# Kernel optimization log

Hardware: AMD Instinct MI355X
Metric: run time of the kernel (lower is better)

Reference implementation:

```python
import jax, jax.numpy as jnp
import numpy as np

B, E, H, A = 16384, 128, 256, 20


def _xavier(key, shape):
    scale = (2.0 / (shape[0] + shape[1])) ** 0.5
    return (jax.random.normal(key, shape, jnp.float32) * scale).astype(jnp.float32)


def setup_inputs() -> dict:
    key = jax.random.key(0)
    ks = jax.random.split(key, 16)
    d = {
        'x1': jax.random.normal(ks[0], (B, E), jnp.float32),
        'x2': jax.random.normal(ks[1], (B, A, E), jnp.float32),
        'h': jax.random.normal(ks[2], (B, H), jnp.float32),
        'c1': jax.random.normal(ks[3], (B, H), jnp.float32),
        'c2': jax.random.normal(ks[4], (B, H), jnp.float32),
    }
    gate_names = ['f', 'i', 'c', 'o']
    for j, n in enumerate(gate_names):
        d[f'W1_{n}'] = _xavier(ks[5 + 2 * j], (H + E, H))
        d[f'W2_{n}'] = _xavier(ks[6 + 2 * j], (H + E, H))
        d[f'b1_{n}'] = jnp.zeros((H,), jnp.float32)
        d[f'b2_{n}'] = jnp.zeros((H,), jnp.float32)
    d['W_attn'] = _xavier(ks[13], (H + 2 * E, 1))
    return d


def reference(x1, x2, h, c1, c2,
              W1_f, W2_f, b1_f, b2_f,
              W1_i, W2_i, b1_i, b2_i,
              W1_c, W2_c, b1_c, b2_c,
              W1_o, W2_o, b1_o, b2_o,
              W_attn):
    hx1 = jnp.concatenate([h, x1], axis=1)                    # [B, H+E]
    # attention: score_a = [h, x1, x2_a] @ W_attn ; split W_attn to vectorize
    base = hx1 @ W_attn[:H + E, 0]                            # [B]
    scores = base[:, None] + jnp.einsum('bae,e->ba', x2, W_attn[H + E:, 0])  # [B, A]
    attn = jax.nn.softmax(scores, axis=1)
    x2m = jnp.einsum('ba,bae->be', attn, x2)                  # [B, E]
    hx2 = jnp.concatenate([h, x2m], axis=1)                   # [B, H+E]

    f1 = jax.nn.sigmoid(hx1 @ W1_f + b1_f)
    f2 = jax.nn.sigmoid(hx2 @ W2_f + b2_f)
    i1 = jax.nn.sigmoid(hx1 @ W1_i + b1_i)
    i2 = jax.nn.sigmoid(hx2 @ W2_i + b2_i)
    c1t = jnp.tanh(hx1 @ W1_c + b1_c)
    c2t = jnp.tanh(hx2 @ W2_c + b2_c)
    c1n = f1 * c1 + i1 * c1t
    c2n = f2 * c2 + i2 * c2t

    o1 = hx1 @ W1_o + b1_o
    o2 = hx2 @ W2_o + b2_o
    # exp(o1)/(exp(o1)+exp(o2)) mixing == softmax over the 2-cell axis (stable form)
    g = jax.nn.softmax(jnp.stack([o1, o2], axis=0), axis=0)
    h_new = g[0] * jnp.tanh(c1n) + g[1] * jnp.tanh(c2n)
    return (h_new, c1n, c2n)
```

## Files before the change

kernel.cpp:

```cpp
#include <hip/hip_runtime.h>
#include <hip/hip_bf16.h>

#define B_SZ 16384
#define E_SZ 128
#define H_SZ 256
#define A_SZ 20
#define K_SZ 384
#define BH   (B_SZ * H_SZ)

typedef __attribute__((ext_vector_type(8))) short  short8v;
typedef __attribute__((ext_vector_type(4))) float  f32x4;
typedef __attribute__((ext_vector_type(2))) float  f32x2;
typedef __attribute__((ext_vector_type(4))) unsigned short ushort4v;
typedef __attribute__((ext_vector_type(2))) unsigned short ushort2v;

__device__ __forceinline__ unsigned short f2bf(float f) {
    union { float f; unsigned u; } v; v.f = f;
    unsigned r = v.u + 0x7fffu + ((v.u >> 16) & 1u);
    return (unsigned short)(r >> 16);
}

__device__ __forceinline__ float wsum(float v) {
    #pragma unroll
    for (int off = 32; off > 0; off >>= 1) v += __shfl_xor(v, off, 64);
    return v;
}

__device__ __forceinline__ float tanh_fast(float x) {
    float cx = fminf(fmaxf(x, -15.f), 15.f);
    float t  = __expf(2.f * cx);
    return (t - 1.f) * __builtin_amdgcn_rcpf(t + 1.f);
}
__device__ __forceinline__ float sigm_fast(float x) {
    float cx = fminf(fmaxf(x, -30.f), 30.f);
    return __builtin_amdgcn_rcpf(1.f + __expf(-cx));
}

struct Ptr8 { const float* p[8]; };

__global__ __launch_bounds__(256) void attn_pack(
    const float* __restrict__ x1, const float* __restrict__ x2,
    const float* __restrict__ h,  const float* __restrict__ wa,
    Ptr8 ws,
    unsigned short* __restrict__ Hb, unsigned short* __restrict__ A1x,
    unsigned short* __restrict__ A2x, unsigned short* __restrict__ Wt)
{
    if (blockIdx.x >= 4096) {
        const int p = blockIdx.x - 4096;
        const int kt = p % 6, nt = (p / 6) & 3, g = p / 24;
        __shared__ float tile[64][65];
        const float* W = ws.p[g];
        const int c = threadIdx.x & 63, r0 = threadIdx.x >> 6;
        #pragma unroll
        for (int i = 0; i < 16; ++i) {
            int r = r0 + 4 * i;
            tile[r][c] = W[(size_t)(kt * 64 + r) * H_SZ + nt * 64 + c];
        }
        __syncthreads();
        #pragma unroll
        for (int i = 0; i < 16; ++i) {
            int rr = r0 + 4 * i;
            const int hcol = nt * 64 + rr;
            const int nn = ((hcol >> 5) << 8) + g * 32 + (hcol & 31);
            Wt[(size_t)nn * K_SZ + kt * 64 + c] = f2bf(tile[c][rr]);
        }
        return;
    }

    const int row  = blockIdx.x * 4 + (threadIdx.x >> 6);
    const int lane = threadIdx.x & 63;

    const f32x4 hv   = *(const f32x4*)(h  + (size_t)row * H_SZ + 4 * lane);
    const f32x2 x1v  = *(const f32x2*)(x1 + (size_t)row * E_SZ + 2 * lane);
    const f32x4 wah  = *(const f32x4*)(wa + 4 * lane);
    const f32x2 wax1 = *(const f32x2*)(wa + H_SZ + 2 * lane);
    const f32x2 wax2 = *(const f32x2*)(wa + H_SZ + E_SZ + 2 * lane);

    float base = hv.x * wah.x + hv.y * wah.y + hv.z * wah.z + hv.w * wah.w
               + x1v.x * wax1.x + x1v.y * wax1.y;

    f32x2 xv[A_SZ];
    float sp[A_SZ];
    const float* x2r = x2 + (size_t)row * A_SZ * E_SZ;
    #pragma unroll
    for (int a = 0; a < A_SZ; ++a) {
        xv[a] = *(const f32x2*)(x2r + a * E_SZ + 2 * lane);
        sp[a] = xv[a].x * wax2.x + xv[a].y * wax2.y;
    }

    base = wsum(base);
    #pragma unroll
    for (int a = 0; a < A_SZ; ++a) sp[a] = wsum(sp[a]) + base;

    float mx = sp[0];
    #pragma unroll
    for (int a = 1; a < A_SZ; ++a) mx = fmaxf(mx, sp[a]);
    float s = 0.0f;
    #pragma unroll
    for (int a = 0; a < A_SZ; ++a) { sp[a] = __expf(sp[a] - mx); s += sp[a]; }
    const float inv = 1.0f / s;

    float m0 = 0.0f, m1 = 0.0f;
    #pragma unroll
    for (int a = 0; a < A_SZ; ++a) { m0 += sp[a] * xv[a].x; m1 += sp[a] * xv[a].y; }
    m0 *= inv; m1 *= inv;

    ushort4v hb;
    hb.x = f2bf(hv.x); hb.y = f2bf(hv.y); hb.z = f2bf(hv.z); hb.w = f2bf(hv.w);
    *(ushort4v*)(Hb + (size_t)row * H_SZ + 4 * lane) = hb;
    ushort2v x1b; x1b.x = f2bf(x1v.x); x1b.y = f2bf(x1v.y);
    *(ushort2v*)(A1x + (size_t)row * E_SZ + 2 * lane) = x1b;
    ushort2v mb; mb.x = f2bf(m0); mb.y = f2bf(m1);
    *(ushort2v*)(A2x + (size_t)row * E_SZ + 2 * lane) = mb;
}

__global__ __launch_bounds__(512, 1) void gemm_ep(
    const unsigned short* __restrict__ Hb, const unsigned short* __restrict__ A1x,
    const unsigned short* __restrict__ A2x, const unsigned short* __restrict__ Wt,
    Ptr8 bias, const float* __restrict__ c1, const float* __restrict__ c2,
    float* __restrict__ out)
{
    __shared__ char smem[131072];
    const int tid = threadIdx.x, w = tid >> 6, lane = tid & 63;
    const int xcd = blockIdx.x & 7, bi = blockIdx.x >> 3;
    const int fr = lane & 15, hi = lane >> 4;
    const int wM = w >> 2, wN = w & 3;
    const int lr = lane >> 3, sl = lane & 7;
    const int hcin = tid & 31, rgrp = tid >> 5;

    auto glds = [&](const unsigned short* src, int dstoff) {
        __builtin_amdgcn_global_load_lds(
            (const __attribute__((address_space(1))) unsigned int*)src,
            (__attribute__((address_space(3))) unsigned int*)(smem + dstoff), 16, 0, 0);
    };
    auto stage = [&](const unsigned short* BpanT, int row0T, int t, int bsel) {
        const int bufb = bsel * 65536;
        #pragma unroll
        for (int j = 0; j < 4; ++j) {
            const int C = j * 64 + w * 8 + lr;
            glds(BpanT + (size_t)C * K_SZ + t * 64 + ((sl ^ (C & 7)) << 3),
                 bufb + 32768 + j * 8192 + w * 1024);
        }
        if (t < 4) {
            #pragma unroll
            for (int i = 0; i < 2; ++i) {
                const int R = i * 64 + w * 8 + lr;
                glds(Hb + (size_t)(row0T + R) * H_SZ + t * 64 + ((sl ^ (R & 7)) << 3),
                     bufb + i * 8192 + w * 1024);
            }
        } else {
            const int ko = (t - 4) * 64;
            #pragma unroll
            for (int i = 0; i < 2; ++i) {
                const int R = i * 64 + w * 8 + lr;
                const int sw = (sl ^ (R & 7)) << 3;
                glds(A1x + (size_t)(row0T + R) * E_SZ + ko + sw,
                     bufb + i * 8192 + w * 1024);
                glds(A2x + (size_t)(row0T + R) * E_SZ + ko + sw,
                     bufb + 16384 + i * 8192 + w * 1024);
            }
        }
    };

    auto tile_coords = [&](int jj, int& row0T, int& hcol0T,
                           const unsigned short*& BpanT) {
        const int hcb = jj & 7, rb = xcd * 16 + (jj >> 3);
        row0T = rb * 128; hcol0T = hcb * 32;
        BpanT = Wt + (size_t)hcb * 256 * K_SZ;
    };

    int row0, hcol0; const unsigned short* Bpan;
    tile_coords(bi * 4, row0, hcol0, Bpan);
    stage(Bpan, row0, 0, 0);

    for (int it = 0; it < 4; ++it) {
        tile_coords(bi * 4 + it, row0, hcol0, Bpan);
        int row0n = 0, hcol0n; const unsigned short* Bpann = nullptr;
        if (it < 3) tile_coords(bi * 4 + it + 1, row0n, hcol0n, Bpann);

        float bia[8], c1p[2][4], c2p[2][4];
        #pragma unroll
        for (int g = 0; g < 8; ++g) bia[g] = bias.p[g][hcol0 + hcin];
        #pragma unroll
        for (int p = 0; p < 2; ++p)
            #pragma unroll
            for (int rr = 0; rr < 4; ++rr) {
                const int R = p * 64 + rgrp * 4 + rr;
                c1p[p][rr] = c1[(size_t)(row0 + R) * H_SZ + hcol0 + hcin];
                c2p[p][rr] = c2[(size_t)(row0 + R) * H_SZ + hcol0 + hcin];
            }

        f32x4 acc[4][4];
        #pragma unroll
        for (int mi = 0; mi < 4; ++mi)
            #pragma unroll
            for (int ni = 0; ni < 4; ++ni) acc[mi][ni] = (f32x4){0.f, 0.f, 0.f, 0.f};

        for (int t = 0; t < 6; ++t) {
            __syncthreads();
            if (t < 5)      stage(Bpan,  row0,  t + 1, (t + 1) & 1);
            else if (it < 3) stage(Bpann, row0n, 0, 0);
            const char* bb = smem + (t & 1) * 65536;
            const int apo = (t >= 4 && wN >= 2) ? 16384 : 0;
            #pragma unroll
            for (int kk = 0; kk < 2; ++kk) {
                short8v af[4], bf[4];
                #pragma unroll
                for (int mi = 0; mi < 4; ++mi) {
                    const int R = wM * 64 + mi * 16 + fr;
                    af[mi] = *(const short8v*)(bb + apo + R * 128 +
                                               ((((kk << 2) + hi) ^ (R & 7)) << 4));
                }
                #pragma unroll
                for (int ni = 0; ni < 4; ++ni) {
                    const int C = wN * 64 + ni * 16 + fr;
                    bf[ni] = *(const short8v*)(bb + 32768 + C * 128 +
                                               ((((kk << 2) + hi) ^ (C & 7)) << 4));
                }
                #pragma unroll
                for (int mi = 0; mi < 4; ++mi)
                    #pragma unroll
                    for (int ni = 0; ni < 4; ++ni)
                        acc[mi][ni] = __builtin_amdgcn_mfma_f32_16x16x32_bf16(
                            af[mi], bf[ni], acc[mi][ni], 0, 0, 0);
            }
        }

        float* gf = (float*)(smem + 65536);
        #pragma unroll
        for (int p = 0; p < 2; ++p) {
            __syncthreads();
            if (wM == p) {
                #pragma unroll
                for (int mi = 0; mi < 4; ++mi)
                    #pragma unroll
                    for (int ni = 0; ni < 4; ++ni)
                        #pragma unroll
                        for (int j = 0; j < 4; ++j) {
                            const int Rl2 = mi * 16 + hi * 4 + j;
                            const int g   = wN * 2 + (ni >> 1);
                            const int hc  = (ni & 1) * 16 + fr;
                            const int hcr = (hc + (((Rl2 >> 2) & 1) << 4)) & 31;
                            gf[(g * 64 + Rl2) * 32 + hcr] = acc[mi][ni][j];
                        }
            }
            __syncthreads();
            #pragma unroll
            for (int rr = 0; rr < 4; ++rr) {
                const int Rl2 = rgrp * 4 + rr;
                const int hcr = (hcin + (((Rl2 >> 2) & 1) << 4)) & 31;
                float G[8];
                #pragma unroll
                for (int g = 0; g < 8; ++g)
                    G[g] = gf[(g * 64 + Rl2) * 32 + hcr] + bia[g];

                const float f1  = sigm_fast(G[0]);
                const float i1  = sigm_fast(G[1]);
                const float c1t = tanh_fast(G[2]);
                const float f2  = sigm_fast(G[4]);
                const float i2  = sigm_fast(G[5]);
                const float c2t = tanh_fast(G[6]);
                const float c1n = f1 * c1p[p][rr] + i1 * c1t;
                const float c2n = f2 * c2p[p][rr] + i2 * c2t;
                const float g0  = sigm_fast(G[3] - G[7]);
                const float th1 = tanh_fast(c1n);
                const float th2 = tanh_fast(c2n);
                const float hn  = th2 + g0 * (th1 - th2);

                const size_t o0 = (size_t)(row0 + p * 64 + Rl2) * H_SZ + hcol0 + hcin;
                out[o0]          = hn;
                out[BH + o0]     = c1n;
                out[2 * BH + o0] = c2n;
            }
        }
    }
}

extern "C" void kernel_launch(void* const* d_in, const int* in_sizes, int n_in,
                              void* d_out, int out_size, void* d_ws, size_t ws_size,
                              hipStream_t stream)
{
    const float* x1 = (const float*)d_in[0];
    const float* x2 = (const float*)d_in[1];
    const float* h  = (const float*)d_in[2];
    const float* c1 = (const float*)d_in[3];
    const float* c2 = (const float*)d_in[4];
    const float* wa = (const float*)d_in[21];

    Ptr8 wptr, bptr;
    wptr.p[0] = (const float*)d_in[5];  wptr.p[1] = (const float*)d_in[9];
    wptr.p[2] = (const float*)d_in[13]; wptr.p[3] = (const float*)d_in[17];
    wptr.p[4] = (const float*)d_in[6];  wptr.p[5] = (const float*)d_in[10];
    wptr.p[6] = (const float*)d_in[14]; wptr.p[7] = (const float*)d_in[18];
    bptr.p[0] = (const float*)d_in[7];  bptr.p[1] = (const float*)d_in[11];
    bptr.p[2] = (const float*)d_in[15]; bptr.p[3] = (const float*)d_in[19];
    bptr.p[4] = (const float*)d_in[8];  bptr.p[5] = (const float*)d_in[12];
    bptr.p[6] = (const float*)d_in[16]; bptr.p[7] = (const float*)d_in[20];

    char* ws = (char*)d_ws;
    unsigned short* Hb  = (unsigned short*)(ws);
    unsigned short* A1x = (unsigned short*)(ws + 8388608);
    unsigned short* A2x = (unsigned short*)(ws + 12582912);
    unsigned short* Wt  = (unsigned short*)(ws + 16777216);

    attn_pack<<<4096 + 192, 256, 0, stream>>>(x1, x2, h, wa, wptr,
                                              Hb, A1x, A2x, Wt);
    gemm_ep<<<256, 512, 0, stream>>>(Hb, A1x, A2x, Wt, bptr, c1, c2, (float*)d_out);
}
```

Measured before the change: 89.37 us.

## Load weight fragments directly into registers instead of staging through LDS

The weight (B operand) tiles are no longer copied into shared memory with global_load_lds. Each wave now reads its own MFMA B fragments straight from global memory into a double-buffered register array, one k-step ahead. Shared-memory buffers shrink to hold only the activation (A) tiles, and the k-loop is fully unrolled so the register buffer indices are static. This cuts LDS traffic and reads for B, but raises VGPR pressure and issues uncoalesced-per-wave global loads, with weights re-fetched by each wM wave pair.

Measured after the change: 120.1 us. 1.34x slower.

```diff
diff --git a/kernel.cpp b/kernel.cpp
--- a/kernel.cpp
+++ b/kernel.cpp
@@ -133,14 +133,8 @@
             (const __attribute__((address_space(1))) unsigned int*)src,
             (__attribute__((address_space(3))) unsigned int*)(smem + dstoff), 16, 0, 0);
     };
-    auto stage = [&](const unsigned short* BpanT, int row0T, int t, int bsel) {
-        const int bufb = bsel * 65536;
-        #pragma unroll
-        for (int j = 0; j < 4; ++j) {
-            const int C = j * 64 + w * 8 + lr;
-            glds(BpanT + (size_t)C * K_SZ + t * 64 + ((sl ^ (C & 7)) << 3),
-                 bufb + 32768 + j * 8192 + w * 1024);
-        }
+    auto stageA = [&](int row0T, int t, int bsel) {
+        const int bufb = bsel * 32768;
         if (t < 4) {
             #pragma unroll
             for (int i = 0; i < 2; ++i) {
@@ -169,9 +163,22 @@
         BpanT = Wt + (size_t)hcb * 256 * K_SZ;
     };
 
+    short8v breg[2][2][4];
+    auto loadB = [&](const unsigned short* BpanT, int t, int par) {
+        #pragma unroll
+        for (int kk = 0; kk < 2; ++kk)
+            #pragma unroll
+            for (int ni = 0; ni < 4; ++ni) {
+                const int C = wN * 64 + ni * 16 + fr;
+                breg[par][kk][ni] = *(const short8v*)(
+                    BpanT + (size_t)C * K_SZ + t * 64 + kk * 32 + hi * 8);
+            }
+    };
+
     int row0, hcol0; const unsigned short* Bpan;
     tile_coords(bi * 4, row0, hcol0, Bpan);
-    stage(Bpan, row0, 0, 0);
+    stageA(row0, 0, 0);
+    loadB(Bpan, 0, 0);
 
     for (int it = 0; it < 4; ++it) {
         tile_coords(bi * 4 + it, row0, hcol0, Bpan);
@@ -196,15 +203,22 @@
             #pragma unroll
             for (int ni = 0; ni < 4; ++ni) acc[mi][ni] = (f32x4){0.f, 0.f, 0.f, 0.f};
 
+        #pragma unroll
         for (int t = 0; t < 6; ++t) {
+            const int cur = t & 1, nxt = cur ^ 1;
             __syncthreads();
-            if (t < 5)      stage(Bpan,  row0,  t + 1, (t + 1) & 1);
-            else if (it < 3) stage(Bpann, row0n, 0, 0);
-            const char* bb = smem + (t & 1) * 65536;
+            if (t < 5) {
+                stageA(row0, t + 1, nxt);
+                loadB(Bpan, t + 1, nxt);
+            } else if (it < 3) {
+                stageA(row0n, 0, 0);
+                loadB(Bpann, 0, 0);
+            }
+            const char* bb = smem + cur * 32768;
             const int apo = (t >= 4 && wN >= 2) ? 16384 : 0;
             #pragma unroll
             for (int kk = 0; kk < 2; ++kk) {
-                short8v af[4], bf[4];
+                short8v af[4];
                 #pragma unroll
                 for (int mi = 0; mi < 4; ++mi) {
                     const int R = wM * 64 + mi * 16 + fr;
@@ -212,17 +226,11 @@
                                                ((((kk << 2) + hi) ^ (R & 7)) << 4));
                 }
                 #pragma unroll
-                for (int ni = 0; ni < 4; ++ni) {
-                    const int C = wN * 64 + ni * 16 + fr;
-                    bf[ni] = *(const short8v*)(bb + 32768 + C * 128 +
-                                               ((((kk << 2) + hi) ^ (C & 7)) << 4));
-                }
-                #pragma unroll
                 for (int mi = 0; mi < 4; ++mi)
                     #pragma unroll
                     for (int ni = 0; ni < 4; ++ni)
                         acc[mi][ni] = __builtin_amdgcn_mfma_f32_16x16x32_bf16(
-                            af[mi], bf[ni], acc[mi][ni], 0, 0, 0);
+                            af[mi], breg[cur][kk][ni], acc[mi][ni], 0, 0, 0);
             }
         }
 
```
